# Kernel tuning notes

Hardware: AMD Instinct MI355X
Metric: run time of the kernel (lower is better)

The kernel has to match this reference:

```python
import jax, jax.numpy as jnp
import numpy as np

BATCH, SEQ, DIM, DSTATE = 8, 2048, 1024, 16


def setup_inputs() -> dict:
    key = jax.random.key(0)
    ks = jax.random.split(key, 8)
    u = jax.random.normal(ks[0], (BATCH, SEQ, DIM), jnp.float32)
    gate = jax.random.normal(ks[1], (BATCH, SEQ, DIM), jnp.float32)
    # parameters (init per module: normal std=0.01 for A_log/B/C, zeros for D)
    A_log = 0.01 * jax.random.normal(ks[2], (DSTATE, DSTATE), jnp.float32)
    B_mat = 0.01 * jax.random.normal(ks[3], (DIM, DSTATE), jnp.float32)
    C_mat = 0.01 * jax.random.normal(ks[4], (DIM, DSTATE), jnp.float32)
    D = jnp.zeros((DIM,), jnp.float32)
    bound = 1.0 / np.sqrt(DIM)  # nn.Linear default init
    dt_w = jax.random.uniform(ks[5], (1, DIM), jnp.float32, -bound, bound)
    dt_b = jax.random.uniform(ks[6], (1,), jnp.float32, -bound, bound)
    return {"u": u, "gate": gate, "A_log": A_log, "B_mat": B_mat,
            "C_mat": C_mat, "D": D, "dt_w": dt_w, "dt_b": dt_b}


def reference(u, gate, A_log, B_mat, C_mat, D, dt_w, dt_b):
    # delta = sigmoid(Linear(gate)) : [B, S, 1] -> [B, S]
    delta = jax.nn.sigmoid(jnp.einsum('bsd,od->bso', gate, dt_w) + dt_b)[..., 0]
    A = -jnp.exp(A_log)                               # [N, N]
    scaled_A = delta[..., None, None] * A             # [B, S, N, N]
    A_exp = jax.scipy.linalg.expm(scaled_A)           # batched matrix exp
    Bu = jnp.einsum('bsd,dn->bsn', u, B_mat)          # [B, S, N]

    def step(h, inp):
        Aexp_t, bu_t = inp                            # [B,N,N], [B,N]
        h = jnp.einsum('bn,bnm->bm', h, Aexp_t) + bu_t
        return h, h

    h0 = jnp.zeros((u.shape[0], DSTATE), u.dtype)
    _, hs = jax.lax.scan(step, h0, (jnp.swapaxes(A_exp, 0, 1), jnp.swapaxes(Bu, 0, 1)))
    hs = jnp.swapaxes(hs, 0, 1)                       # [B, S, N]
    y = jnp.einsum('bsn,dn->bsd', hs, C_mat) + D * u  # [B, S, D]
    return y
```

## Files before the change

kernel.cpp:

```cpp
#include <hip/hip_runtime.h>

#define BATCH  8
#define SEQ    2048
#define DIMSZ  1024
#define NST    16
#define LCH    32
#define CPB    (SEQ / LCH)
#define NCHUNK (BATCH * CPB)
#define NCHEB  32
#define PI_F   3.14159265358979f

typedef __attribute__((ext_vector_type(8))) short bf16x8;
typedef __attribute__((ext_vector_type(4))) float f32x4;

static __device__ __forceinline__ unsigned short f2bf(float f) {
    unsigned u = __builtin_bit_cast(unsigned, f);
    unsigned r = (u + 0x7FFFu + ((u >> 16) & 1u)) >> 16;
    return (unsigned short)r;
}
static __device__ __forceinline__ float bf2f(unsigned short h) {
    unsigned u = ((unsigned)h) << 16;
    return __builtin_bit_cast(float, u);
}

__global__ __launch_bounds__(256) void k0_sa_delta(
    const float* __restrict__ A_log, const float* __restrict__ gate,
    const float* __restrict__ dt_w, const float* __restrict__ dt_b,
    float* __restrict__ Fn, float* __restrict__ delta)
{
    __shared__ float Xs[16 * 17];
    __shared__ float Ts[16 * 17];
    const int tid  = threadIdx.x;
    const int lane = tid & 63;
    const int w    = tid >> 6;
    const int g    = blockIdx.x;

    if (g >= 32) {
        const int tok  = (g - 32) * 4 + w;
        const float* gp = gate + (size_t)tok * DIMSZ;
        float s = 0.f;
#pragma unroll
        for (int i = 0; i < 4; ++i) {
            const float4 gv = *(const float4*)(gp   + i * 256 + lane * 4);
            const float4 wv = *(const float4*)(dt_w + i * 256 + lane * 4);
            s = fmaf(gv.x, wv.x, s); s = fmaf(gv.y, wv.y, s);
            s = fmaf(gv.z, wv.z, s); s = fmaf(gv.w, wv.w, s);
        }
#pragma unroll
        for (int off = 32; off >= 1; off >>= 1)
            s += __shfl_xor(s, off, 64);
        if (lane == 0)
            delta[tok] = 1.0f / (1.0f + expf(-(s + dt_b[0])));
        return;
    }

    const int i = tid >> 4, j = tid & 15;
    const float th = (2.f * g + 1.f) * (PI_F / 64.f);
    const float dl = 0.5f * (1.f + cosf(th));
    const float a  = -expf(A_log[tid]);
    const float x  = dl * a * (1.0f / 64.0f);
    Xs[i*17 + j] = x;
    Ts[i*17 + j] = x;
    float S = x + (i == j ? 1.0f : 0.0f);
    __syncthreads();
#pragma unroll
    for (int k = 2; k <= 8; ++k) {
        float nt = 0.f;
#pragma unroll
        for (int kk = 0; kk < 16; ++kk)
            nt = fmaf(Ts[i*17 + kk], Xs[kk*17 + j], nt);
        nt *= (1.0f / (float)k);
        S += nt;
        __syncthreads();
        Ts[i*17 + j] = nt;
        __syncthreads();
    }
#pragma unroll
    for (int r = 0; r < 6; ++r) {
        __syncthreads();
        Ts[i*17 + j] = S;
        __syncthreads();
        float nt = 0.f;
#pragma unroll
        for (int kk = 0; kk < 16; ++kk)
            nt = fmaf(Ts[i*17 + kk], Ts[kk*17 + j], nt);
        S = nt;
    }
    Fn[(size_t)g * 256 + tid] = S;
}

__global__ __launch_bounds__(256) void sB_setup(
    const float* __restrict__ Fn, const float* __restrict__ B_mat,
    float* __restrict__ Gt,
    unsigned short* __restrict__ Bfh, unsigned short* __restrict__ Bfl)
{
    const int tid = threadIdx.x;
    const int blk = blockIdx.x;
    if (blk < NCHEB) {
        const int m = blk;
        float acc = 0.f;
        for (int k = 0; k < NCHEB; ++k) {
            const float th = (2.f * k + 1.f) * (PI_F / 64.f);
            acc = fmaf(Fn[(size_t)k * 256 + tid], cosf(m * th), acc);
        }
        const float sc = (m == 0) ? (1.f / 32.f) : (2.f / 32.f);
        Gt[(size_t)tid * NCHEB + m] = acc * sc;
    } else {
        const int idx0 = (blk - NCHEB) * 2048;
        for (int t = 0; t < 8; ++t) {
            const int idx = idx0 + t * 256 + tid;
            const int j  = idx & 7;
            const int l  = (idx >> 3) & 63;
            const int ks = idx >> 9;
            const int k  = ks * 32 + ((l >> 4) << 3) + j;
            const int n  = l & 15;
            float bv = B_mat[(size_t)k * 16 + n];
            unsigned short h = f2bf(bv);
            Bfh[idx] = h;
            Bfl[idx] = f2bf(bv - bf2f(h));
        }
    }
}

__global__ __launch_bounds__(512, 4) void kBA4(
    const float* __restrict__ u,
    const unsigned short* __restrict__ Bfh, const unsigned short* __restrict__ Bfl,
    const float* __restrict__ Gt, const float* __restrict__ delta,
    float* __restrict__ Bu, float* __restrict__ P, float* __restrict__ e)
{
    __shared__ float smem[8704];
    __shared__ float Bus[LCH * NST];
    __shared__ float dl[LCH];
    __shared__ float sd[1];
    __shared__ float Ps[16 * 17];
    const int tid  = threadIdx.x;
    const int lane = tid & 63;
    const int w    = tid >> 6;
    const size_t gI = blockIdx.x;
    const int tok0 = (int)gI * 32;
    const int qk   = w & 3;
    const int tt   = w >> 2;
    const int q    = lane >> 4;
    const int r    = lane & 15;

    if (tid < LCH) dl[tid] = delta[gI * LCH + tid];

    const uint4* bh = (const uint4*)Bfh;
    const uint4* bl = (const uint4*)Bfl;

    const float* up = u + (size_t)(tok0 + tt * 16 + r) * DIMSZ + qk * 256 + q * 8;

    f32x4 acc0 = {0.f, 0.f, 0.f, 0.f};
    f32x4 acc1 = {0.f, 0.f, 0.f, 0.f};
#pragma unroll
    for (int c = 0; c < 8; c += 2) {
        const float4 a0 = *(const float4*)(up + c * 32);
        const float4 a1 = *(const float4*)(up + c * 32 + 4);
        const float4 b0 = *(const float4*)(up + (c + 1) * 32);
        const float4 b1 = *(const float4*)(up + (c + 1) * 32 + 4);
        const uint4 FH0 = bh[(qk * 8 + c) * 64 + lane];
        const uint4 FL0 = bl[(qk * 8 + c) * 64 + lane];
        const uint4 FH1 = bh[(qk * 8 + c + 1) * 64 + lane];
        const uint4 FL1 = bl[(qk * 8 + c + 1) * 64 + lane];
        __builtin_amdgcn_sched_barrier(0);
        const float fu0[8] = {a0.x, a0.y, a0.z, a0.w, a1.x, a1.y, a1.z, a1.w};
        const float fu1[8] = {b0.x, b0.y, b0.z, b0.w, b1.x, b1.y, b1.z, b1.w};
        bf16x8 uh0, ul0, uh1, ul1;
#pragma unroll
        for (int i = 0; i < 8; ++i) {
            unsigned short h = f2bf(fu0[i]);
            uh0[i] = (short)h; ul0[i] = (short)f2bf(fu0[i] - bf2f(h));
            h = f2bf(fu1[i]);
            uh1[i] = (short)h; ul1[i] = (short)f2bf(fu1[i] - bf2f(h));
        }
        const bf16x8 Bh0 = __builtin_bit_cast(bf16x8, FH0);
        const bf16x8 Bl0 = __builtin_bit_cast(bf16x8, FL0);
        const bf16x8 Bh1 = __builtin_bit_cast(bf16x8, FH1);
        const bf16x8 Bl1 = __builtin_bit_cast(bf16x8, FL1);
        acc0 = __builtin_amdgcn_mfma_f32_16x16x32_bf16(uh0, Bh0, acc0, 0, 0, 0);
        acc1 = __builtin_amdgcn_mfma_f32_16x16x32_bf16(uh1, Bh1, acc1, 0, 0, 0);
        acc0 = __builtin_amdgcn_mfma_f32_16x16x32_bf16(uh0, Bl0, acc0, 0, 0, 0);
        acc1 = __builtin_amdgcn_mfma_f32_16x16x32_bf16(uh1, Bl1, acc1, 0, 0, 0);
        acc0 = __builtin_amdgcn_mfma_f32_16x16x32_bf16(ul0, Bh0, acc0, 0, 0, 0);
        acc1 = __builtin_amdgcn_mfma_f32_16x16x32_bf16(ul1, Bh1, acc1, 0, 0, 0);
    }
    f32x4 acc;
#pragma unroll
    for (int rr = 0; rr < 4; ++rr) acc[rr] = acc0[rr] + acc1[rr];

    float* red = smem;
#pragma unroll
    for (int rr = 0; rr < 4; ++rr)
        red[w * 256 + (q * 4 + rr) * 16 + r] = acc[rr];
    __syncthreads();
    const int rb = (tid >> 8) * 1024 + (tid & 255);
    const float bv = red[rb] + red[rb + 256] + red[rb + 512] + red[rb + 768];
    Bu[gI * 512 + tid] = bv;
    Bus[tid] = bv;

    const int el = tid & 255;
    float gr[NCHEB];
    {
        const float4* gp = (const float4*)(Gt + (size_t)el * NCHEB);
#pragma unroll
        for (int qq = 0; qq < NCHEB / 4; ++qq) {
            float4 v = gp[qq];
            gr[qq*4+0] = v.x; gr[qq*4+1] = v.y; gr[qq*4+2] = v.z; gr[qq*4+3] = v.w;
        }
    }
    __syncthreads();
    if (tid == 0) {
        float s = 0.f;
        for (int t = 0; t < LCH; ++t) s += dl[t];
        sd[0] = s;
    }
    const int tgrp = tid >> 8;
    for (int t = tgrp * 16; t < tgrp * 16 + 16; ++t) {
        const float x = 2.f * dl[t] - 1.f;
        float accm = fmaf(gr[1], x, gr[0]);
        float tm2 = 1.f, tm1 = x;
#pragma unroll
        for (int m = 2; m < NCHEB; ++m) {
            const float tm = fmaf(2.f * x, tm1, -tm2);
            accm = fmaf(gr[m], tm, accm);
            tm2 = tm1; tm1 = tm;
        }
        smem[t * 272 + (el >> 4) * 17 + (el & 15)] = accm;
    }
    __syncthreads();
    float S;
    {
        const float xp = 2.f * (sd[0] * (1.f / LCH)) - 1.f;
        float accm = fmaf(gr[1], xp, gr[0]);
        float tm2 = 1.f, tm1 = xp;
#pragma unroll
        for (int m = 2; m < NCHEB; ++m) {
            const float tm = fmaf(2.f * xp, tm1, -tm2);
            accm = fmaf(gr[m], tm, accm);
            tm2 = tm1; tm1 = tm;
        }
        S = accm;
    }
    const int i = el >> 4, j = el & 15;
#pragma unroll
    for (int rr = 0; rr < 5; ++rr) {
        if (tid < 256) Ps[i*17 + j] = S;
        __syncthreads();
        float ns = 0.f;
#pragma unroll
        for (int k = 0; k < 16; ++k)
            ns = fmaf(Ps[i*17 + k], Ps[k*17 + j], ns);
        __syncthreads();
        S = ns;
    }
    if (tid < 256) P[gI * 256 + tid] = S;
    if (tid < 64) {
        const int gq = tid >> 4, jj = tid & 15, i0 = gq * 4;
        float h = 0.f;
        for (int t = 0; t < LCH; ++t) {
            float pp = 0.f;
#pragma unroll
            for (int m = 0; m < 4; ++m)
                pp = fmaf(__shfl(h, gq * 20 + m, 64),
                          smem[t * 272 + (i0 + m) * 17 + jj], pp);
            pp += __shfl_xor(pp, 16, 64);
            pp += __shfl_xor(pp, 32, 64);
            h = Bus[t * 16 + jj] + pp;
        }
        if (gq == 0) e[gI * NST + jj] = h;
    }
}

__global__ __launch_bounds__(256) void k4_scan(
    const float* __restrict__ P, const float* __restrict__ e,
    float* __restrict__ hin)
{
    __shared__ float Pl[32 * 272];
    __shared__ float el[32 * NST];
    const int tid = threadIdx.x;
    const int b = blockIdx.x;
    float h = 0.f;
    for (int half = 0; half < 2; ++half) {
        const int c0 = half * 32;
        for (int idx = tid; idx < 32*256; idx += 256) {
            const int c = idx >> 8, ij = idx & 255, i = ij >> 4, jj = ij & 15;
            Pl[c*272 + i*17 + jj] = P[((size_t)(b*CPB + c0 + c)) * 256 + ij];
        }
        for (int idx = tid; idx < 32*NST; idx += 256)
            el[idx] = e[((size_t)(b*CPB + c0)) * NST + idx];
        __syncthreads();
        if (tid < 64) {
            const int gq = tid >> 4, j = tid & 15, i0 = gq * 4;
            for (int c = 0; c < 32; ++c) {
                if (tid < 16) hin[((size_t)(b*CPB + c0 + c)) * NST + j] = h;
                float pp = 0.f;
#pragma unroll
                for (int m = 0; m < 4; ++m)
                    pp = fmaf(__shfl(h, gq * 20 + m, 64),
                              Pl[c*272 + (i0 + m)*17 + j], pp);
                pp += __shfl_xor(pp, 16, 64);
                pp += __shfl_xor(pp, 32, 64);
                h = el[c*16 + j] + pp;
            }
        }
        __syncthreads();
    }
}

__global__ __launch_bounds__(512, 4) void k5b(
    const float* __restrict__ Gt, const float* __restrict__ delta,
    const float* __restrict__ Bu, const float* __restrict__ hin,
    const float* __restrict__ u, const float* __restrict__ C_mat,
    const float* __restrict__ D, float* __restrict__ y)
{
    __shared__ float Mlds[32 * 272];
    __shared__ float Bus[LCH * NST];
    __shared__ float dl[LCH];
    __shared__ __align__(16) float Hs[LCH * NST];
    const int tid = threadIdx.x;
    const size_t g = blockIdx.x;
    const int el = tid & 255;
    const int tgrp = tid >> 8;
    if (tid < LCH) dl[tid] = delta[g * LCH + tid];
    Bus[tid] = Bu[g * 512 + tid];
    float gr[NCHEB];
    {
        const float4* gp = (const float4*)(Gt + (size_t)el * NCHEB);
#pragma unroll
        for (int qq = 0; qq < NCHEB / 4; ++qq) {
            float4 v = gp[qq];
            gr[qq*4+0] = v.x; gr[qq*4+1] = v.y; gr[qq*4+2] = v.z; gr[qq*4+3] = v.w;
        }
    }
    __syncthreads();
    for (int t = tgrp * 16; t < tgrp * 16 + 16; ++t) {
        const float x = 2.f * dl[t] - 1.f;
        float accm = fmaf(gr[1], x, gr[0]);
        float tm2 = 1.f, tm1 = x;
#pragma unroll
        for (int m = 2; m < NCHEB; ++m) {
            const float tm = fmaf(2.f * x, tm1, -tm2);
            accm = fmaf(gr[m], tm, accm);
            tm2 = tm1; tm1 = tm;
        }
        Mlds[t * 272 + (el >> 4) * 17 + (el & 15)] = accm;
    }
    __syncthreads();
    if (tid < 64) {
        const int gq = tid >> 4, jj = tid & 15, i0 = gq * 4;
        float h = hin[g * NST + jj];
        for (int t = 0; t < LCH; ++t) {
            float pp = 0.f;
#pragma unroll
            for (int m = 0; m < 4; ++m)
                pp = fmaf(__shfl(h, gq * 20 + m, 64),
                          Mlds[t * 272 + (i0 + m) * 17 + jj], pp);
            pp += __shfl_xor(pp, 16, 64);
            pp += __shfl_xor(pp, 32, 64);
            h = Bus[t * 16 + jj] + pp;
            if (gq == 0) Hs[t * 16 + jj] = h;
        }
    }
    __syncthreads();
    const int d0 = el * 4;
    float4 cr[4][4];
#pragma unroll
    for (int r = 0; r < 4; ++r)
#pragma unroll
        for (int qq = 0; qq < 4; ++qq)
            cr[r][qq] = ((const float4*)C_mat)[(d0 + r) * 4 + qq];
    const float4 dv = ((const float4*)D)[el];
    const bool dnz = (dv.x != 0.f) || (dv.y != 0.f) || (dv.z != 0.f) || (dv.w != 0.f);
    for (int t = tgrp * 16; t < tgrp * 16 + 16; ++t) {
        const size_t row = (g * LCH + t) * DIMSZ;
        float y0 = 0.f, y1 = 0.f, y2 = 0.f, y3 = 0.f;
        if (dnz) {
            const float4 uv = ((const float4*)(u + row))[el];
            y0 = dv.x * uv.x; y1 = dv.y * uv.y; y2 = dv.z * uv.z; y3 = dv.w * uv.w;
        }
#pragma unroll
        for (int qq = 0; qq < 4; ++qq) {
            const float4 hq = *((const float4*)&Hs[t*16 + qq*4]);
            y0 = fmaf(hq.x, cr[0][qq].x, y0); y0 = fmaf(hq.y, cr[0][qq].y, y0);
            y0 = fmaf(hq.z, cr[0][qq].z, y0); y0 = fmaf(hq.w, cr[0][qq].w, y0);
            y1 = fmaf(hq.x, cr[1][qq].x, y1); y1 = fmaf(hq.y, cr[1][qq].y, y1);
            y1 = fmaf(hq.z, cr[1][qq].z, y1); y1 = fmaf(hq.w, cr[1][qq].w, y1);
            y2 = fmaf(hq.x, cr[2][qq].x, y2); y2 = fmaf(hq.y, cr[2][qq].y, y2);
            y2 = fmaf(hq.z, cr[2][qq].z, y2); y2 = fmaf(hq.w, cr[2][qq].w, y2);
            y3 = fmaf(hq.x, cr[3][qq].x, y3); y3 = fmaf(hq.y, cr[3][qq].y, y3);
            y3 = fmaf(hq.z, cr[3][qq].z, y3); y3 = fmaf(hq.w, cr[3][qq].w, y3);
        }
        float4 ov; ov.x = y0; ov.y = y1; ov.z = y2; ov.w = y3;
        ((float4*)(y + row))[el] = ov;
    }
}

extern "C" void kernel_launch(void* const* d_in, const int* in_sizes, int n_in,
                              void* d_out, int out_size, void* d_ws, size_t ws_size,
                              hipStream_t stream)
{
    const float* u     = (const float*)d_in[0];
    const float* gate  = (const float*)d_in[1];
    const float* A_log = (const float*)d_in[2];
    const float* B_mat = (const float*)d_in[3];
    const float* C_mat = (const float*)d_in[4];
    const float* D     = (const float*)d_in[5];
    const float* dt_w  = (const float*)d_in[6];
    const float* dt_b  = (const float*)d_in[7];
    float* y = (float*)d_out;

    float* ws = (float*)d_ws;
    size_t o = 0;
    float* Fn    = ws + o; o += 32 * 256;
    float* Gt    = ws + o; o += 256 * NCHEB;
    float* delta = ws + o; o += (size_t)BATCH * SEQ;
    float* Bu    = ws + o; o += (size_t)BATCH * SEQ * NST;
    float* P     = ws + o; o += (size_t)NCHUNK * 256;
    float* e     = ws + o; o += (size_t)NCHUNK * NST;
    float* hin   = ws + o; o += (size_t)NCHUNK * NST;
    unsigned short* Bfh = (unsigned short*)(ws + o); o += 8192;
    unsigned short* Bfl = (unsigned short*)(ws + o); o += 8192;

    k0_sa_delta<<<BATCH * SEQ / 4 + 32, 256, 0, stream>>>(
        A_log, gate, dt_w, dt_b, Fn, delta);
    sB_setup<<<NCHEB + 8, 256, 0, stream>>>(Fn, B_mat, Gt, Bfh, Bfl);
    kBA4    <<<NCHUNK, 512, 0, stream>>>(u, Bfh, Bfl, Gt, delta, Bu, P, e);
    k4_scan <<<BATCH,  256, 0, stream>>>(P, e, hin);
    k5b     <<<NCHUNK, 512, 0, stream>>>(Gt, delta, Bu, hin, u, C_mat, D, y);
}
```

Baseline: 236.6 us.

## Fuse setup and scan kernels to cut five launches down to three

Moves the bf16 split of B_mat into the first kernel. Every chunk block of the second kernel now recomputes the Chebyshev coefficient table from Fn itself, and block 0 writes it out for the last kernel. The separate inter-chunk scan kernel is removed: each output block replays the carry recurrence over all earlier chunks in its batch, loading the next chunk's values ahead of use. This removes two launches and a serial 8-block kernel, at the cost of redundant per-block Chebyshev work and a prefix replay of up to 63 chunks per block.

```diff
diff --git a/kernel.cpp b/kernel.cpp
--- a/kernel.cpp
+++ b/kernel.cpp
@@ -23,10 +23,12 @@
     return __builtin_bit_cast(float, u);
 }
 
-__global__ __launch_bounds__(256) void k0_sa_delta(
+__global__ __launch_bounds__(256) void k0_sa_delta_bf(
     const float* __restrict__ A_log, const float* __restrict__ gate,
     const float* __restrict__ dt_w, const float* __restrict__ dt_b,
-    float* __restrict__ Fn, float* __restrict__ delta)
+    const float* __restrict__ B_mat,
+    float* __restrict__ Fn, float* __restrict__ delta,
+    unsigned short* __restrict__ Bfh, unsigned short* __restrict__ Bfl)
 {
     __shared__ float Xs[16 * 17];
     __shared__ float Ts[16 * 17];
@@ -35,78 +37,8 @@
     const int w    = tid >> 6;
     const int g    = blockIdx.x;
 
-    if (g >= 32) {
-        const int tok  = (g - 32) * 4 + w;
-        const float* gp = gate + (size_t)tok * DIMSZ;
-        float s = 0.f;
-#pragma unroll
-        for (int i = 0; i < 4; ++i) {
-            const float4 gv = *(const float4*)(gp   + i * 256 + lane * 4);
-            const float4 wv = *(const float4*)(dt_w + i * 256 + lane * 4);
-            s = fmaf(gv.x, wv.x, s); s = fmaf(gv.y, wv.y, s);
-            s = fmaf(gv.z, wv.z, s); s = fmaf(gv.w, wv.w, s);
-        }
-#pragma unroll
-        for (int off = 32; off >= 1; off >>= 1)
-            s += __shfl_xor(s, off, 64);
-        if (lane == 0)
-            delta[tok] = 1.0f / (1.0f + expf(-(s + dt_b[0])));
-        return;
-    }
-
-    const int i = tid >> 4, j = tid & 15;
-    const float th = (2.f * g + 1.f) * (PI_F / 64.f);
-    const float dl = 0.5f * (1.f + cosf(th));
-    const float a  = -expf(A_log[tid]);
-    const float x  = dl * a * (1.0f / 64.0f);
-    Xs[i*17 + j] = x;
-    Ts[i*17 + j] = x;
-    float S = x + (i == j ? 1.0f : 0.0f);
-    __syncthreads();
-#pragma unroll
-    for (int k = 2; k <= 8; ++k) {
-        float nt = 0.f;
-#pragma unroll
-        for (int kk = 0; kk < 16; ++kk)
-            nt = fmaf(Ts[i*17 + kk], Xs[kk*17 + j], nt);
-        nt *= (1.0f / (float)k);
-        S += nt;
-        __syncthreads();
-        Ts[i*17 + j] = nt;
-        __syncthreads();
-    }
-#pragma unroll
-    for (int r = 0; r < 6; ++r) {
-        __syncthreads();
-        Ts[i*17 + j] = S;
-        __syncthreads();
-        float nt = 0.f;
-#pragma unroll
-        for (int kk = 0; kk < 16; ++kk)
-            nt = fmaf(Ts[i*17 + kk], Ts[kk*17 + j], nt);
-        S = nt;
-    }
-    Fn[(size_t)g * 256 + tid] = S;
-}
-
-__global__ __launch_bounds__(256) void sB_setup(
-    const float* __restrict__ Fn, const float* __restrict__ B_mat,
-    float* __restrict__ Gt,
-    unsigned short* __restrict__ Bfh, unsigned short* __restrict__ Bfl)
-{
-    const int tid = threadIdx.x;
-    const int blk = blockIdx.x;
-    if (blk < NCHEB) {
-        const int m = blk;
-        float acc = 0.f;
-        for (int k = 0; k < NCHEB; ++k) {
-            const float th = (2.f * k + 1.f) * (PI_F / 64.f);
-            acc = fmaf(Fn[(size_t)k * 256 + tid], cosf(m * th), acc);
-        }
-        const float sc = (m == 0) ? (1.f / 32.f) : (2.f / 32.f);
-        Gt[(size_t)tid * NCHEB + m] = acc * sc;
-    } else {
-        const int idx0 = (blk - NCHEB) * 2048;
+    if (g >= 4128) {
+        const int idx0 = (g - 4128) * 2048;
         for (int t = 0; t < 8; ++t) {
             const int idx = idx0 + t * 256 + tid;
             const int j  = idx & 7;
@@ -119,14 +51,68 @@
             Bfh[idx] = h;
             Bfl[idx] = f2bf(bv - bf2f(h));
         }
-    }
-}
-
-__global__ __launch_bounds__(512, 4) void kBA4(
+        return;
+    }
+    if (g >= 32) {
+        const int tok  = (g - 32) * 4 + w;
+        const float* gp = gate + (size_t)tok * DIMSZ;
+        float s = 0.f;
+#pragma unroll
+        for (int i = 0; i < 4; ++i) {
+            const float4 gv = *(const float4*)(gp   + i * 256 + lane * 4);
+            const float4 wv = *(const float4*)(dt_w + i * 256 + lane * 4);
+            s = fmaf(gv.x, wv.x, s); s = fmaf(gv.y, wv.y, s);
+            s = fmaf(gv.z, wv.z, s); s = fmaf(gv.w, wv.w, s);
+        }
+#pragma unroll
+        for (int off = 32; off >= 1; off >>= 1)
+            s += __shfl_xor(s, off, 64);
+        if (lane == 0)
+            delta[tok] = 1.0f / (1.0f + expf(-(s + dt_b[0])));
+        return;
+    }
+
+    const int i = tid >> 4, j = tid & 15;
+    const float th = (2.f * g + 1.f) * (PI_F / 64.f);
+    const float dl = 0.5f * (1.f + cosf(th));
+    const float a  = -expf(A_log[tid]);
+    const float x  = dl * a * (1.0f / 64.0f);
+    Xs[i*17 + j] = x;
+    Ts[i*17 + j] = x;
+    float S = x + (i == j ? 1.0f : 0.0f);
+    __syncthreads();
+#pragma unroll
+    for (int k = 2; k <= 8; ++k) {
+        float nt = 0.f;
+#pragma unroll
+        for (int kk = 0; kk < 16; ++kk)
+            nt = fmaf(Ts[i*17 + kk], Xs[kk*17 + j], nt);
+        nt *= (1.0f / (float)k);
+        S += nt;
+        __syncthreads();
+        Ts[i*17 + j] = nt;
+        __syncthreads();
+    }
+#pragma unroll
+    for (int r = 0; r < 6; ++r) {
+        __syncthreads();
+        Ts[i*17 + j] = S;
+        __syncthreads();
+        float nt = 0.f;
+#pragma unroll
+        for (int kk = 0; kk < 16; ++kk)
+            nt = fmaf(Ts[i*17 + kk], Ts[kk*17 + j], nt);
+        S = nt;
+    }
+    Fn[(size_t)g * 256 + tid] = S;
+}
+
+__global__ __launch_bounds__(512, 4) void kBA5(
     const float* __restrict__ u,
     const unsigned short* __restrict__ Bfh, const unsigned short* __restrict__ Bfl,
-    const float* __restrict__ Gt, const float* __restrict__ delta,
-    float* __restrict__ Bu, float* __restrict__ P, float* __restrict__ e)
+    const float* __restrict__ Fn, const float* __restrict__ delta,
+    float* __restrict__ Gt, float* __restrict__ Bu,
+    float* __restrict__ P, float* __restrict__ e)
 {
     __shared__ float smem[8704];
     __shared__ float Bus[LCH * NST];
@@ -200,12 +186,32 @@
 
     const int el = tid & 255;
     float gr[NCHEB];
-    {
-        const float4* gp = (const float4*)(Gt + (size_t)el * NCHEB);
+#pragma unroll
+    for (int m = 0; m < NCHEB; ++m) gr[m] = 0.f;
+    for (int k = 0; k < NCHEB; ++k) {
+        const float f  = Fn[(size_t)k * 256 + el];
+        const float th = (2.f * k + 1.f) * (PI_F / 64.f);
+        const float ck = cosf(th);
+        float cm2 = 1.f, cm1 = ck;
+        gr[0] += f;
+        gr[1] = fmaf(f, ck, gr[1]);
+#pragma unroll
+        for (int m = 2; m < NCHEB; ++m) {
+            const float cm = fmaf(2.f * ck, cm1, -cm2);
+            gr[m] = fmaf(f, cm, gr[m]);
+            cm2 = cm1; cm1 = cm;
+        }
+    }
+#pragma unroll
+    for (int m = 0; m < NCHEB; ++m)
+        gr[m] *= (m == 0) ? (1.f / 32.f) : (2.f / 32.f);
+    if (gI == 0 && tid < 256) {
+        float4* gp = (float4*)(Gt + (size_t)el * NCHEB);
 #pragma unroll
         for (int qq = 0; qq < NCHEB / 4; ++qq) {
-            float4 v = gp[qq];
-            gr[qq*4+0] = v.x; gr[qq*4+1] = v.y; gr[qq*4+2] = v.z; gr[qq*4+3] = v.w;
+            float4 v; v.x = gr[qq*4+0]; v.y = gr[qq*4+1];
+            v.z = gr[qq*4+2]; v.w = gr[qq*4+3];
+            gp[qq] = v;
         }
     }
     __syncthreads();
@@ -271,47 +277,12 @@
     }
 }
 
-__global__ __launch_bounds__(256) void k4_scan(
-    const float* __restrict__ P, const float* __restrict__ e,
-    float* __restrict__ hin)
-{
-    __shared__ float Pl[32 * 272];
-    __shared__ float el[32 * NST];
-    const int tid = threadIdx.x;
-    const int b = blockIdx.x;
-    float h = 0.f;
-    for (int half = 0; half < 2; ++half) {
-        const int c0 = half * 32;
-        for (int idx = tid; idx < 32*256; idx += 256) {
-            const int c = idx >> 8, ij = idx & 255, i = ij >> 4, jj = ij & 15;
-            Pl[c*272 + i*17 + jj] = P[((size_t)(b*CPB + c0 + c)) * 256 + ij];
-        }
-        for (int idx = tid; idx < 32*NST; idx += 256)
-            el[idx] = e[((size_t)(b*CPB + c0)) * NST + idx];
-        __syncthreads();
-        if (tid < 64) {
-            const int gq = tid >> 4, j = tid & 15, i0 = gq * 4;
-            for (int c = 0; c < 32; ++c) {
-                if (tid < 16) hin[((size_t)(b*CPB + c0 + c)) * NST + j] = h;
-                float pp = 0.f;
-#pragma unroll
-                for (int m = 0; m < 4; ++m)
-                    pp = fmaf(__shfl(h, gq * 20 + m, 64),
-                              Pl[c*272 + (i0 + m)*17 + j], pp);
-                pp += __shfl_xor(pp, 16, 64);
-                pp += __shfl_xor(pp, 32, 64);
-                h = el[c*16 + j] + pp;
-            }
-        }
-        __syncthreads();
-    }
-}
-
-__global__ __launch_bounds__(512, 4) void k5b(
+__global__ __launch_bounds__(512, 4) void k5c(
     const float* __restrict__ Gt, const float* __restrict__ delta,
-    const float* __restrict__ Bu, const float* __restrict__ hin,
-    const float* __restrict__ u, const float* __restrict__ C_mat,
-    const float* __restrict__ D, float* __restrict__ y)
+    const float* __restrict__ Bu, const float* __restrict__ P,
+    const float* __restrict__ e, const float* __restrict__ u,
+    const float* __restrict__ C_mat, const float* __restrict__ D,
+    float* __restrict__ y)
 {
     __shared__ float Mlds[32 * 272];
     __shared__ float Bus[LCH * NST];
@@ -348,7 +319,55 @@
     __syncthreads();
     if (tid < 64) {
         const int gq = tid >> 4, jj = tid & 15, i0 = gq * 4;
-        float h = hin[g * NST + jj];
+        const int cend = (int)(g & (CPB - 1));
+        const size_t base = (g >> 6) * (size_t)CPB;
+        float h = 0.f;
+        float pA0 = 0.f, pA1 = 0.f, pA2 = 0.f, pA3 = 0.f, eA = 0.f;
+        float pB0 = 0.f, pB1 = 0.f, pB2 = 0.f, pB3 = 0.f, eB = 0.f;
+        if (cend > 0) {
+            const float* Pp = P + base * 256;
+            pA0 = Pp[(i0+0)*16 + jj]; pA1 = Pp[(i0+1)*16 + jj];
+            pA2 = Pp[(i0+2)*16 + jj]; pA3 = Pp[(i0+3)*16 + jj];
+            eA  = e[base * NST + jj];
+        }
+        int cc = 0;
+        while (cc < cend) {
+            if (cc + 1 < cend) {
+                const float* Pp = P + (base + cc + 1) * 256;
+                pB0 = Pp[(i0+0)*16 + jj]; pB1 = Pp[(i0+1)*16 + jj];
+                pB2 = Pp[(i0+2)*16 + jj]; pB3 = Pp[(i0+3)*16 + jj];
+                eB  = e[(base + cc + 1) * NST + jj];
+            }
+            {
+                float pp = 0.f;
+                pp = fmaf(__shfl(h, gq * 20 + 0, 64), pA0, pp);
+                pp = fmaf(__shfl(h, gq * 20 + 1, 64), pA1, pp);
+                pp = fmaf(__shfl(h, gq * 20 + 2, 64), pA2, pp);
+                pp = fmaf(__shfl(h, gq * 20 + 3, 64), pA3, pp);
+                pp += __shfl_xor(pp, 16, 64);
+                pp += __shfl_xor(pp, 32, 64);
+                h = eA + pp;
+            }
+            ++cc;
+            if (cc >= cend) break;
+            if (cc + 1 < cend) {
+                const float* Pp = P + (base + cc + 1) * 256;
+                pA0 = Pp[(i0+0)*16 + jj]; pA1 = Pp[(i0+1)*16 + jj];
+                pA2 = Pp[(i0+2)*16 + jj]; pA3 = Pp[(i0+3)*16 + jj];
+                eA  = e[(base + cc + 1) * NST + jj];
+            }
+            {
+                float pp = 0.f;
+                pp = fmaf(__shfl(h, gq * 20 + 0, 64), pB0, pp);
+                pp = fmaf(__shfl(h, gq * 20 + 1, 64), pB1, pp);
+                pp = fmaf(__shfl(h, gq * 20 + 2, 64), pB2, pp);
+                pp = fmaf(__shfl(h, gq * 20 + 3, 64), pB3, pp);
+                pp += __shfl_xor(pp, 16, 64);
+                pp += __shfl_xor(pp, 32, 64);
+                h = eB + pp;
+            }
+            ++cc;
+        }
         for (int t = 0; t < LCH; ++t) {
             float pp = 0.f;
 #pragma unroll
@@ -417,14 +436,11 @@
     float* Bu    = ws + o; o += (size_t)BATCH * SEQ * NST;
     float* P     = ws + o; o += (size_t)NCHUNK * 256;
     float* e     = ws + o; o += (size_t)NCHUNK * NST;
-    float* hin   = ws + o; o += (size_t)NCHUNK * NST;
     unsigned short* Bfh = (unsigned short*)(ws + o); o += 8192;
     unsigned short* Bfl = (unsigned short*)(ws + o); o += 8192;
 
-    k0_sa_delta<<<BATCH * SEQ / 4 + 32, 256, 0, stream>>>(
-        A_log, gate, dt_w, dt_b, Fn, delta);
-    sB_setup<<<NCHEB + 8, 256, 0, stream>>>(Fn, B_mat, Gt, Bfh, Bfl);
-    kBA4    <<<NCHUNK, 512, 0, stream>>>(u, Bfh, Bfl, Gt, delta, Bu, P, e);
-    k4_scan <<<BATCH,  256, 0, stream>>>(P, e, hin);
-    k5b     <<<NCHUNK, 512, 0, stream>>>(Gt, delta, Bu, hin, u, C_mat, D, y);
-}
+    k0_sa_delta_bf<<<BATCH * SEQ / 4 + 32 + 8, 256, 0, stream>>>(
+        A_log, gate, dt_w, dt_b, B_mat, Fn, delta, Bfh, Bfl);
+    kBA5<<<NCHUNK, 512, 0, stream>>>(u, Bfh, Bfl, Fn, delta, Gt, Bu, P, e);
+    k5c <<<NCHUNK, 512, 0, stream>>>(Gt, delta, Bu, P, e, u, C_mat, D, y);
+}
```

Measured after the change: 238.6 us. Within noise of the previous version (+0.9%).
